# Kernel tuning notes

Hardware: AMD Instinct MI355X
Metric: run time of the kernel (lower is better)

Reference implementation:

```python
import jax, jax.numpy as jnp
import numpy as np

NEUMANN_TERMS = 6
EPS_PASSTHROUGH = 1e-6  # hn_config.GRADIENT_PASSTHROUGH_EPSILON (assumed)


def _cayley_neumann(W, terms=NEUMANN_TERMS):
    """Cayley transform U = (I - A)^{-1} (I + A) with A = skew(W),
    where (I - A)^{-1} is approximated by the truncated Neumann series
    sum_{k=0}^{terms-1} A^k."""
    A = 0.5 * (W - W.T)                       # skew-symmetric generator
    I = jnp.eye(W.shape[0], dtype=W.dtype)
    S = I
    P = I
    for _ in range(terms - 1):                # small fixed loop (neumann_terms)
        P = P @ A
        S = S + P
    return S @ (I + A)


def _quantum_rotation(h, theta):
    """Parametric quantum rotation activation: rotate adjacent feature pairs
    by angle theta (norm-preserving, replaces ReLU/GELU)."""
    N, d = h.shape
    hp = h.reshape(N, d // 2, 2)
    c, s = jnp.cos(theta), jnp.sin(theta)
    x0, x1 = hp[..., 0], hp[..., 1]
    r0 = c * x0 - s * x1
    r1 = s * x0 + c * x1
    return jnp.stack([r0, r1], axis=-1).reshape(N, d)


def setup_inputs() -> dict:
    key = jax.random.key(0)
    k1, k2, k3 = jax.random.split(key, 3)
    N, d_model, d_ff = 65536, 1024, 1024
    inputs = jax.random.normal(k1, (N, d_model), dtype=jnp.float32)
    # Orthogonal initializer with gain 0.1 (as in build())
    q1 = jnp.linalg.qr(jax.random.normal(k2, (d_ff, d_model), dtype=jnp.float32))[0]
    q2 = jnp.linalg.qr(jax.random.normal(k3, (d_model, d_ff), dtype=jnp.float32))[0]
    u1_weights = 0.1 * q1
    u2_weights = 0.1 * q2
    activation_angle = jnp.float32(0.7854)  # pi/4 initializer
    return {"inputs": inputs, "u1_weights": u1_weights,
            "u2_weights": u2_weights, "activation_angle": activation_angle}


def reference(inputs, u1_weights, u2_weights, activation_angle):
    U1 = _cayley_neumann(u1_weights)          # [d_ff, d_model]
    U2 = _cayley_neumann(u2_weights)          # [d_model, d_ff]
    h = inputs @ U1.T                         # [N, d_ff]
    h = _quantum_rotation(h, activation_angle)
    out = h @ U2.T                            # [N, d_model]
    # gradient passthrough term from call()
    passthrough = (jnp.mean(u1_weights) * EPS_PASSTHROUGH
                   + jnp.mean(u2_weights) * EPS_PASSTHROUGH
                   + activation_angle * EPS_PASSTHROUGH)
    return out + passthrough
```

## Files before the change

kernel.cpp:

```cpp
#include <hip/hip_runtime.h>
#include <hip/hip_bf16.h>
#include <stdint.h>


#define MM (1024 * 1024)

typedef __attribute__((ext_vector_type(4))) float f32x4;
typedef __attribute__((ext_vector_type(8))) short bf16x8;

__device__ __forceinline__ ushort f2bf(float f) {
  uint32_t u = __builtin_bit_cast(uint32_t, f);
  u += 0x7FFFu + ((u >> 16) & 1u);
  return (ushort)(u >> 16);
}

__device__ __forceinline__ void gld_lds16(const ushort* g, ushort* l) {
  __builtin_amdgcn_global_load_lds(
      (const __attribute__((address_space(1))) unsigned int*)g,
      (__attribute__((address_space(3))) unsigned int*)l, 16, 0, 0);
}

#define STAGE(GS, LB, BUF, H, KT)                                    \
  do {                                                               \
    const ushort* g_ = (GS) + (size_t)((H)*128) * K + (size_t)(KT)*64; \
    ushort* d_ = (LB) + (BUF)*32768 + (H)*128 * 64;                  \
    gld_lds16(g_, d_);                                               \
    gld_lds16(g_ + (size_t)64 * K, d_ + 64 * 64);                    \
  } while (0)

#define LDA(MH, BUF)                                                    \
  do {                                                                  \
    _Pragma("unroll") for (int ti = 0; ti < 4; ++ti) {                  \
      const ushort* p_ = rdA + (BUF)*32768 + ((MH)*64 + ti * 16 + lr) * 64; \
      af[ti][0] = *(const bf16x8*)(p_ + (pcol0 >> 1));                  \
      af[ti][1] = *(const bf16x8*)(p_ + (pcol1 >> 1));                  \
    }                                                                   \
  } while (0)

#define LDB(NH, BUF)                                                    \
  do {                                                                  \
    _Pragma("unroll") for (int tj = 0; tj < 2; ++tj) {                  \
      const ushort* p_ = rdB + (BUF)*32768 + ((NH)*32 + tj * 16 + lr) * 64; \
      bfr[tj][0] = *(const bf16x8*)(p_ + (pcol0 >> 1));                 \
      bfr[tj][1] = *(const bf16x8*)(p_ + (pcol1 >> 1));                 \
    }                                                                   \
  } while (0)

#define MFMA16(MH, NH)                                                  \
  do {                                                                  \
    __builtin_amdgcn_s_setprio(1);                                      \
    _Pragma("unroll") for (int m_ = 0; m_ < 4; ++m_)                    \
    _Pragma("unroll") for (int n_ = 0; n_ < 2; ++n_)                    \
    _Pragma("unroll") for (int ks_ = 0; ks_ < 2; ++ks_)                 \
      acc[(MH)*4 + m_][(NH)*2 + n_] =                                   \
          __builtin_amdgcn_mfma_f32_16x16x32_bf16(                      \
              af[m_][ks_], bfr[n_][ks_], acc[(MH)*4 + m_][(NH)*2 + n_], \
              0, 0, 0);                                                 \
    __builtin_amdgcn_s_setprio(0);                                      \
  } while (0)

#define CFENCE asm volatile("" ::: "memory")
#define SBAR                                  \
  do {                                        \
    CFENCE;                                   \
    __builtin_amdgcn_s_barrier();             \
    __builtin_amdgcn_sched_barrier(0);        \
  } while (0)

__global__ __launch_bounds__(512, 2) void gemm256(
    const ushort* __restrict__ X, const ushort* __restrict__ Y,
    float* __restrict__ o32, ushort* __restrict__ o16, int M, int N, int K,
    int mode, const float* __restrict__ theta_p,
    const float* __restrict__ sums) {
  extern __shared__ ushort lds[];

  const int tid = threadIdx.x;
  const int wave = tid >> 6, lane = tid & 63;

  const int nwg = gridDim.x * gridDim.y;
  const int lin = blockIdx.y * gridDim.x + blockIdx.x;
  const int wgid = (lin & 7) * (nwg >> 3) + (lin >> 3);
  const int bn = wgid & 3;
  const int bm = wgid >> 2;

  const int wrow = wave >> 2;
  const int wcol = wave & 3;

  const int srow = wave * 8 + (lane >> 3);
  const int scol = (((lane & 7) ^ ((lane >> 3) & 7)) << 3);
  const ushort* Xs = X + (size_t)(bm * 256 + srow) * K + scol;
  const ushort* Ys = Y + (size_t)(bn * 256 + srow) * K + scol;
  ushort* stA = lds + wave * 8 * 64;
  ushort* stB = lds + 16384 + wave * 8 * 64;

  const int lr = lane & 15;
  const int kqb = (lane >> 4) << 4;
  const int swz = (lr & 7) << 4;
  const int pcol0 = (0 + kqb) ^ swz;
  const int pcol1 = (64 + kqb) ^ swz;
  const ushort* rdA = lds + wrow * 128 * 64;
  const ushort* rdB = lds + 16384 + wcol * 64 * 64;

  f32x4 acc[8][4] = {};
  bf16x8 af[4][2], bfr[2][2];

  const int NT = K >> 6;

  STAGE(Xs, stA, 0, 0, 0);
  STAGE(Xs, stA, 0, 1, 0);
  STAGE(Ys, stB, 0, 0, 0);
  STAGE(Ys, stB, 0, 1, 0);

  for (int t = 0; t < NT; ++t) {
    const int cur = t & 1, nxt = cur ^ 1;
    const bool pf = (t + 1 < NT);
    if (pf) {
      STAGE(Xs, stA, nxt, 0, t + 1);
      asm volatile("s_waitcnt vmcnt(2)" ::: "memory");
    } else {
      asm volatile("s_waitcnt vmcnt(0)" ::: "memory");
    }
    SBAR;
    LDA(0, cur);
    LDB(0, cur);
    MFMA16(0, 0);
    SBAR;
    LDB(1, cur);
    if (pf) STAGE(Xs, stA, nxt, 1, t + 1);
    SBAR;
    MFMA16(0, 1);
    SBAR;
    LDA(1, cur);
    if (pf) STAGE(Ys, stB, nxt, 0, t + 1);
    SBAR;
    MFMA16(1, 1);
    SBAR;
    LDB(0, cur);
    if (pf) STAGE(Ys, stB, nxt, 1, t + 1);
    SBAR;
    MFMA16(1, 0);
    SBAR;
  }

  const int q4 = (lane >> 4) * 4;
  const int rbase = bm * 256 + wrow * 128;
  const int cbase = bn * 256 + wcol * 64;
  if (mode == 1) {
    float th = *theta_p, s, c;
    __sincosf(th, &s, &c);
    const float ssgn = (lane & 1) ? s : -s;
#pragma unroll
    for (int fi = 0; fi < 8; ++fi)
#pragma unroll
      for (int r = 0; r < 4; ++r) {
        const size_t row = (size_t)(rbase + fi * 16 + q4 + r);
        ushort* Orow = o16 + row * N;
#pragma unroll
        for (int fj = 0; fj < 4; ++fj) {
          float v = acc[fi][fj][r];
          float w = __shfl_xor(v, 1);
          Orow[cbase + fj * 16 + lr] = f2bf(c * v + ssgn * w);
        }
      }
  } else {
    const float pt = 1e-6f * (sums[0] * (1.0f / 1048576.0f) +
                              sums[1] * (1.0f / 1048576.0f) + *theta_p);
#pragma unroll
    for (int fi = 0; fi < 8; ++fi)
#pragma unroll
      for (int r = 0; r < 4; ++r) {
        const size_t row = (size_t)(rbase + fi * 16 + q4 + r);
        float* Orow = o32 + row * N;
#pragma unroll
        for (int fj = 0; fj < 4; ++fj)
          Orow[cbase + fj * 16 + lr] = acc[fi][fj][r] + pt;
      }
  }
}

__global__ __launch_bounds__(256, 2) void gemm_bt(
    const ushort* __restrict__ X0, const ushort* __restrict__ X1,
    const ushort* __restrict__ Y0, const ushort* __restrict__ Y1,
    float* __restrict__ o32, ushort* __restrict__ o16,
    ushort* __restrict__ o16b, const float* __restrict__ aux, int M, int N,
    int K, int mode, const float* __restrict__ theta_p,
    const float* __restrict__ sums) {
  __shared__ ushort lA[128 * 32];
  __shared__ ushort lB[128 * 32];

  const int tid = threadIdx.x;
  const int wave = tid >> 6, lane = tid & 63;
  const int bz = blockIdx.z;
  const int job = bz >> 1, mi = bz & 1;

  const int nwg = gridDim.x * gridDim.y;
  const int lin = blockIdx.y * gridDim.x + blockIdx.x;
  const int swzb = (lin & 7) * (nwg >> 3) + (lin >> 3);
  const int bn = swzb & 7;
  const int bm = swzb >> 3;

  const ushort* X = (job ? X1 : X0) + (size_t)mi * MM;
  const ushort* Y = (job ? Y1 : Y0) + (size_t)mi * MM;

  const ushort* Xg = X + (size_t)(bm * 128 + (tid >> 2)) * K + (tid & 3) * 8;
  const ushort* Yg = Y + (size_t)(bn * 128 + (tid >> 2)) * K + (tid & 3) * 8;
  ushort* lAw = lA + wave * 512;
  ushort* lBw = lB + wave * 512;

  const int wm = (wave & 1) * 64;
  const int wn = (wave >> 1) * 64;
  const int lr = lane & 15;
  const int kq = (lane >> 4) * 8;

  f32x4 acc[4][4] = {};

  for (int k0 = 0; k0 < K; k0 += 32) {
    __syncthreads();
    gld_lds16(Xg + k0, lAw);
    gld_lds16(Xg + k0 + (size_t)64 * K, lAw + 64 * 32);
    gld_lds16(Yg + k0, lBw);
    gld_lds16(Yg + k0 + (size_t)64 * K, lBw + 64 * 32);
    __syncthreads();

    bf16x8 afv[4], bfg[4];
#pragma unroll
    for (int t = 0; t < 4; ++t) {
      afv[t] = *(const bf16x8*)(lA + (wm + t * 16 + lr) * 32 + kq);
      bfg[t] = *(const bf16x8*)(lB + (wn + t * 16 + lr) * 32 + kq);
    }
#pragma unroll
    for (int ti = 0; ti < 4; ++ti)
#pragma unroll
      for (int tj = 0; tj < 4; ++tj)
        acc[ti][tj] = __builtin_amdgcn_mfma_f32_16x16x32_bf16(
            afv[ti], bfg[tj], acc[ti][tj], 0, 0, 0);
  }

  const int q4 = (lane >> 4) * 4;
  float* O = o32 + (size_t)bz * MM;
  ushort* P0 = (mode >= 3) ? o16 + (size_t)bz * MM : nullptr;
  ushort* P1 = (mode == 4) ? o16b + (size_t)bz * MM : nullptr;
  const float* Ax = (mode == 4) ? aux + (size_t)bz * MM : nullptr;
#pragma unroll
  for (int ti = 0; ti < 4; ++ti)
#pragma unroll
    for (int r = 0; r < 4; ++r) {
      const int row = bm * 128 + wm + ti * 16 + q4 + r;
      const size_t base = (size_t)row * N;
#pragma unroll
      for (int tj = 0; tj < 4; ++tj) {
        const int col = bn * 128 + wn + tj * 16 + lr;
        const float v = acc[ti][tj][r];
        O[base + col] = v;
        if (mode == 3) {
          P0[base + col] = f2bf(-v);
        } else if (mode == 4) {
          P0[base + col] = f2bf(v);
          const float diag = (row == col) ? 1.f : 0.f;
          P1[base + col] = f2bf(diag - Ax[base + col] + v);
        }
      }
    }
}

__global__ __launch_bounds__(256) void prep_a(const float* __restrict__ W1,
                                              const float* __restrict__ W2,
                                              ushort* __restrict__ Abf,
                                              float* __restrict__ sums) {
  __shared__ float sT[32][33];
  const int z = blockIdx.z;
  const float* W = z ? W2 : W1;
  ushort* A = Abf + (size_t)z * MM;
  const int r0 = blockIdx.y * 32, c0 = blockIdx.x * 32;
  const int x = threadIdx.x, y = threadIdx.y;

#pragma unroll
  for (int k = 0; k < 4; ++k)
    sT[y + 8 * k][x] = W[(size_t)(c0 + y + 8 * k) * 1024 + r0 + x];
  __syncthreads();

  float lsum = 0.f;
#pragma unroll
  for (int k = 0; k < 4; ++k) {
    int i = y + 8 * k;
    float w = W[(size_t)(r0 + i) * 1024 + c0 + x];
    lsum += w;
    A[(size_t)(r0 + i) * 1024 + c0 + x] = f2bf(0.5f * (w - sT[x][i]));
  }
#pragma unroll
  for (int off = 32; off > 0; off >>= 1) lsum += __shfl_down(lsum, off);
  if (((y * 32 + x) & 63) == 0) atomicAdd(&sums[z], lsum);
}

__global__ __launch_bounds__(256) void cvt_x(const float* __restrict__ x,
                                             ushort* __restrict__ xb) {
  const size_t i = (size_t)blockIdx.x * 256 + threadIdx.x;
  float4 v = ((const float4*)x)[i];
  ushort4 o;
  o.x = f2bf(v.x);
  o.y = f2bf(v.y);
  o.z = f2bf(v.z);
  o.w = f2bf(v.w);
  ((ushort4*)xb)[i] = o;
}

__global__ __launch_bounds__(256) void ew(const float* __restrict__ S1,
                                          const float* __restrict__ S2,
                                          const float* __restrict__ S3,
                                          const float* __restrict__ S4,
                                          ushort* __restrict__ O0) {
  const int idx = blockIdx.x * 256 + threadIdx.x;
  const int local = idx & (MM - 1);
  const float diag = ((local >> 10) == (local & 1023)) ? 1.f : 0.f;
  O0[idx] =
      f2bf(diag - 2.f * S1[idx] + 2.f * S2[idx] + 2.f * S3[idx] + S4[idx]);
}

extern "C" void kernel_launch(void* const* d_in, const int* in_sizes, int n_in,
                              void* d_out, int out_size, void* d_ws,
                              size_t ws_size, hipStream_t stream) {
  const float* xin = (const float*)d_in[0];
  const float* w1 = (const float*)d_in[1];
  const float* w2 = (const float*)d_in[2];
  const float* th = (const float*)d_in[3];
  float* out = (float*)d_out;

  char* w = (char*)d_ws;
  float* sums = (float*)w;
  ushort* Abf = (ushort*)(w + 256);
  ushort* Bbf = Abf + 2 * MM;
  ushort* B2bf = Bbf + 2 * MM;
  ushort* Fbf = B2bf + 2 * MM;
  ushort* Ubf = Fbf + 2 * MM;
  float* S1 = (float*)(Ubf + 2 * MM);
  float* S2 = S1 + 2 * MM;
  float* S34 = S2 + 2 * MM;
  ushort* xbf = (ushort*)(S34 + 4 * MM);
  ushort* hbf = xbf + (size_t)65536 * 1024;

  static bool inited = false;
  if (!inited) {
    (void)hipFuncSetAttribute((const void*)gemm256,
                              hipFuncAttributeMaxDynamicSharedMemorySize,
                              131072);
    inited = true;
  }

  hipMemsetAsync(sums, 0, 2 * sizeof(float), stream);

  prep_a<<<dim3(32, 32, 2), dim3(32, 8), 0, stream>>>(w1, w2, Abf, sums);
  cvt_x<<<65536, 256, 0, stream>>>(xin, xbf);

  gemm_bt<<<dim3(8, 8, 2), 256, 0, stream>>>(Abf, Abf, Abf, Abf, S1, Bbf,
                                             nullptr, nullptr, 1024, 1024,
                                             1024, 3, th, sums);
  gemm_bt<<<dim3(8, 8, 2), 256, 0, stream>>>(Bbf, Bbf, Bbf, Bbf, S2, B2bf, Fbf,
                                             S1, 1024, 1024, 1024, 4, th,
                                             sums);
  gemm_bt<<<dim3(8, 8, 4), 256, 0, stream>>>(Abf, B2bf, Fbf, Bbf, S34, nullptr,
                                             nullptr, nullptr, 1024, 1024,
                                             1024, 0, th, sums);
  ew<<<8192, 256, 0, stream>>>(S1, S2, S34, S34 + 2 * MM, Ubf);

  gemm256<<<dim3(4, 256, 1), 512, 131072, stream>>>(
      xbf, Ubf, nullptr, hbf, 65536, 1024, 1024, 1, th, sums);
  gemm256<<<dim3(4, 256, 1), 512, 131072, stream>>>(
      hbf, Ubf + MM, out, nullptr, 65536, 1024, 1024, 2, th, sums);
}
```

Measured before the change: 913.6 us.

## Refactor Neumann weight GEMM chain to one product and batch gemm256 prefetch

The Cayley/Neumann weight construction is re-expressed algebraically so the final U comes from a single product G·F, with the identity and scale terms folded into the GEMM epilogues. This drops one 4-batch GEMM, the elementwise combine kernel and several fp32 intermediates. Separately, the main 256-tile GEMM now issues all next-tile global-to-LDS loads at the top of each iteration instead of interleaving them between MFMA phases. That gives the loads more lead time but bunches memory traffic into one burst per iteration.

```diff
diff --git a/kernel.cpp b/kernel.cpp
--- a/kernel.cpp
+++ b/kernel.cpp
@@ -13,6 +13,10 @@
   u += 0x7FFFu + ((u >> 16) & 1u);
   return (ushort)(u >> 16);
 }
+__device__ __forceinline__ float bf2f(ushort h) {
+  uint32_t u = ((uint32_t)h) << 16;
+  return __builtin_bit_cast(float, u);
+}
 
 __device__ __forceinline__ void gld_lds16(const ushort* g, ushort* l) {
   __builtin_amdgcn_global_load_lds(
@@ -20,30 +24,30 @@
       (__attribute__((address_space(3))) unsigned int*)l, 16, 0, 0);
 }
 
-#define STAGE(GS, LB, BUF, H, KT)                                    \
-  do {                                                               \
+#define STAGE(GS, LB, BUF, H, KT)                                      \
+  do {                                                                 \
     const ushort* g_ = (GS) + (size_t)((H)*128) * K + (size_t)(KT)*64; \
-    ushort* d_ = (LB) + (BUF)*32768 + (H)*128 * 64;                  \
-    gld_lds16(g_, d_);                                               \
-    gld_lds16(g_ + (size_t)64 * K, d_ + 64 * 64);                    \
-  } while (0)
-
-#define LDA(MH, BUF)                                                    \
-  do {                                                                  \
-    _Pragma("unroll") for (int ti = 0; ti < 4; ++ti) {                  \
+    ushort* d_ = (LB) + (BUF)*32768 + (H)*128 * 64;                    \
+    gld_lds16(g_, d_);                                                 \
+    gld_lds16(g_ + (size_t)64 * K, d_ + 64 * 64);                      \
+  } while (0)
+
+#define LDA(MH, BUF)                                                        \
+  do {                                                                      \
+    _Pragma("unroll") for (int ti = 0; ti < 4; ++ti) {                      \
       const ushort* p_ = rdA + (BUF)*32768 + ((MH)*64 + ti * 16 + lr) * 64; \
-      af[ti][0] = *(const bf16x8*)(p_ + (pcol0 >> 1));                  \
-      af[ti][1] = *(const bf16x8*)(p_ + (pcol1 >> 1));                  \
-    }                                                                   \
-  } while (0)
-
-#define LDB(NH, BUF)                                                    \
-  do {                                                                  \
-    _Pragma("unroll") for (int tj = 0; tj < 2; ++tj) {                  \
+      af[ti][0] = *(const bf16x8*)(p_ + (pcol0 >> 1));                      \
+      af[ti][1] = *(const bf16x8*)(p_ + (pcol1 >> 1));                      \
+    }                                                                       \
+  } while (0)
+
+#define LDB(NH, BUF)                                                        \
+  do {                                                                      \
+    _Pragma("unroll") for (int tj = 0; tj < 2; ++tj) {                      \
       const ushort* p_ = rdB + (BUF)*32768 + ((NH)*32 + tj * 16 + lr) * 64; \
-      bfr[tj][0] = *(const bf16x8*)(p_ + (pcol0 >> 1));                 \
-      bfr[tj][1] = *(const bf16x8*)(p_ + (pcol1 >> 1));                 \
-    }                                                                   \
+      bfr[tj][0] = *(const bf16x8*)(p_ + (pcol0 >> 1));                     \
+      bfr[tj][1] = *(const bf16x8*)(p_ + (pcol1 >> 1));                     \
+    }                                                                       \
   } while (0)
 
 #define MFMA16(MH, NH)                                                  \
@@ -60,11 +64,11 @@
   } while (0)
 
 #define CFENCE asm volatile("" ::: "memory")
-#define SBAR                                  \
-  do {                                        \
-    CFENCE;                                   \
-    __builtin_amdgcn_s_barrier();             \
-    __builtin_amdgcn_sched_barrier(0);        \
+#define SBAR                           \
+  do {                                 \
+    CFENCE;                            \
+    __builtin_amdgcn_s_barrier();      \
+    __builtin_amdgcn_sched_barrier(0); \
   } while (0)
 
 __global__ __launch_bounds__(512, 2) void gemm256(
@@ -113,10 +117,12 @@
 
   for (int t = 0; t < NT; ++t) {
     const int cur = t & 1, nxt = cur ^ 1;
-    const bool pf = (t + 1 < NT);
-    if (pf) {
+    if (t + 1 < NT) {
       STAGE(Xs, stA, nxt, 0, t + 1);
-      asm volatile("s_waitcnt vmcnt(2)" ::: "memory");
+      STAGE(Xs, stA, nxt, 1, t + 1);
+      STAGE(Ys, stB, nxt, 0, t + 1);
+      STAGE(Ys, stB, nxt, 1, t + 1);
+      asm volatile("s_waitcnt vmcnt(8)" ::: "memory");
     } else {
       asm volatile("s_waitcnt vmcnt(0)" ::: "memory");
     }
@@ -126,17 +132,14 @@
     MFMA16(0, 0);
     SBAR;
     LDB(1, cur);
-    if (pf) STAGE(Xs, stA, nxt, 1, t + 1);
     SBAR;
     MFMA16(0, 1);
     SBAR;
     LDA(1, cur);
-    if (pf) STAGE(Ys, stB, nxt, 0, t + 1);
     SBAR;
     MFMA16(1, 1);
     SBAR;
     LDB(0, cur);
-    if (pf) STAGE(Ys, stB, nxt, 1, t + 1);
     SBAR;
     MFMA16(1, 0);
     SBAR;
@@ -179,19 +182,17 @@
 }
 
 __global__ __launch_bounds__(256, 2) void gemm_bt(
-    const ushort* __restrict__ X0, const ushort* __restrict__ X1,
-    const ushort* __restrict__ Y0, const ushort* __restrict__ Y1,
+    const ushort* __restrict__ X0, const ushort* __restrict__ Y0,
     float* __restrict__ o32, ushort* __restrict__ o16,
-    ushort* __restrict__ o16b, const float* __restrict__ aux, int M, int N,
-    int K, int mode, const float* __restrict__ theta_p,
-    const float* __restrict__ sums) {
+    ushort* __restrict__ o16b, const float* __restrict__ auxf,
+    const ushort* __restrict__ auxb, int M, int N, int K, int mode,
+    const float* __restrict__ theta_p, const float* __restrict__ sums) {
   __shared__ ushort lA[128 * 32];
   __shared__ ushort lB[128 * 32];
 
   const int tid = threadIdx.x;
   const int wave = tid >> 6, lane = tid & 63;
-  const int bz = blockIdx.z;
-  const int job = bz >> 1, mi = bz & 1;
+  const int mi = blockIdx.z & 1;
 
   const int nwg = gridDim.x * gridDim.y;
   const int lin = blockIdx.y * gridDim.x + blockIdx.x;
@@ -199,8 +200,8 @@
   const int bn = swzb & 7;
   const int bm = swzb >> 3;
 
-  const ushort* X = (job ? X1 : X0) + (size_t)mi * MM;
-  const ushort* Y = (job ? Y1 : Y0) + (size_t)mi * MM;
+  const ushort* X = X0 + (size_t)mi * MM;
+  const ushort* Y = Y0 + (size_t)mi * MM;
 
   const ushort* Xg = X + (size_t)(bm * 128 + (tid >> 2)) * K + (tid & 3) * 8;
   const ushort* Yg = Y + (size_t)(bn * 128 + (tid >> 2)) * K + (tid & 3) * 8;
@@ -237,10 +238,12 @@
   }
 
   const int q4 = (lane >> 4) * 4;
-  float* O = o32 + (size_t)bz * MM;
-  ushort* P0 = (mode >= 3) ? o16 + (size_t)bz * MM : nullptr;
-  ushort* P1 = (mode == 4) ? o16b + (size_t)bz * MM : nullptr;
-  const float* Ax = (mode == 4) ? aux + (size_t)bz * MM : nullptr;
+  const size_t zoff = (size_t)mi * MM;
+  float* O = (mode == 3) ? o32 + zoff : nullptr;
+  ushort* P0 = o16 + zoff;
+  ushort* P1 = (mode == 3) ? o16b + zoff : nullptr;
+  const float* Ax = (mode == 4) ? auxf + zoff : nullptr;
+  const ushort* Ab = (mode == 3) ? auxb + zoff : nullptr;
 #pragma unroll
   for (int ti = 0; ti < 4; ++ti)
 #pragma unroll
@@ -251,13 +254,15 @@
       for (int tj = 0; tj < 4; ++tj) {
         const int col = bn * 128 + wn + tj * 16 + lr;
         const float v = acc[ti][tj][r];
-        O[base + col] = v;
+        const float diag = (row == col) ? 1.f : 0.f;
         if (mode == 3) {
+          O[base + col] = v;
           P0[base + col] = f2bf(-v);
+          P1[base + col] = f2bf(diag + 2.f * bf2f(Ab[base + col]) - v);
         } else if (mode == 4) {
+          P0[base + col] = f2bf(diag - Ax[base + col] + v);
+        } else {
           P0[base + col] = f2bf(v);
-          const float diag = (row == col) ? 1.f : 0.f;
-          P1[base + col] = f2bf(diag - Ax[base + col] + v);
         }
       }
     }
@@ -304,18 +309,6 @@
   ((ushort4*)xb)[i] = o;
 }
 
-__global__ __launch_bounds__(256) void ew(const float* __restrict__ S1,
-                                          const float* __restrict__ S2,
-                                          const float* __restrict__ S3,
-                                          const float* __restrict__ S4,
-                                          ushort* __restrict__ O0) {
-  const int idx = blockIdx.x * 256 + threadIdx.x;
-  const int local = idx & (MM - 1);
-  const float diag = ((local >> 10) == (local & 1023)) ? 1.f : 0.f;
-  O0[idx] =
-      f2bf(diag - 2.f * S1[idx] + 2.f * S2[idx] + 2.f * S3[idx] + S4[idx]);
-}
-
 extern "C" void kernel_launch(void* const* d_in, const int* in_sizes, int n_in,
                               void* d_out, int out_size, void* d_ws,
                               size_t ws_size, hipStream_t stream) {
@@ -329,13 +322,11 @@
   float* sums = (float*)w;
   ushort* Abf = (ushort*)(w + 256);
   ushort* Bbf = Abf + 2 * MM;
-  ushort* B2bf = Bbf + 2 * MM;
-  ushort* Fbf = B2bf + 2 * MM;
+  ushort* Gbf = Bbf + 2 * MM;
+  ushort* Fbf = Gbf + 2 * MM;
   ushort* Ubf = Fbf + 2 * MM;
   float* S1 = (float*)(Ubf + 2 * MM);
-  float* S2 = S1 + 2 * MM;
-  float* S34 = S2 + 2 * MM;
-  ushort* xbf = (ushort*)(S34 + 4 * MM);
+  ushort* xbf = (ushort*)(S1 + 2 * MM);
   ushort* hbf = xbf + (size_t)65536 * 1024;
 
   static bool inited = false;
@@ -351,16 +342,15 @@
   prep_a<<<dim3(32, 32, 2), dim3(32, 8), 0, stream>>>(w1, w2, Abf, sums);
   cvt_x<<<65536, 256, 0, stream>>>(xin, xbf);
 
-  gemm_bt<<<dim3(8, 8, 2), 256, 0, stream>>>(Abf, Abf, Abf, Abf, S1, Bbf,
+  gemm_bt<<<dim3(8, 8, 2), 256, 0, stream>>>(Abf, Abf, S1, Bbf, Gbf, nullptr,
+                                             Abf, 1024, 1024, 1024, 3, th,
+                                             sums);
+  gemm_bt<<<dim3(8, 8, 2), 256, 0, stream>>>(Bbf, Bbf, nullptr, Fbf, nullptr,
+                                             S1, nullptr, 1024, 1024, 1024, 4,
+                                             th, sums);
+  gemm_bt<<<dim3(8, 8, 2), 256, 0, stream>>>(Gbf, Fbf, nullptr, Ubf, nullptr,
                                              nullptr, nullptr, 1024, 1024,
-                                             1024, 3, th, sums);
-  gemm_bt<<<dim3(8, 8, 2), 256, 0, stream>>>(Bbf, Bbf, Bbf, Bbf, S2, B2bf, Fbf,
-                                             S1, 1024, 1024, 1024, 4, th,
-                                             sums);
-  gemm_bt<<<dim3(8, 8, 4), 256, 0, stream>>>(Abf, B2bf, Fbf, Bbf, S34, nullptr,
-                                             nullptr, nullptr, 1024, 1024,
-                                             1024, 0, th, sums);
-  ew<<<8192, 256, 0, stream>>>(S1, S2, S34, S34 + 2 * MM, Ubf);
+                                             1024, 5, th, sums);
 
   gemm256<<<dim3(4, 256, 1), 512, 131072, stream>>>(
       xbf, Ubf, nullptr, hbf, 65536, 1024, 1024, 1, th, sums);
```

After: 959.4 us. 1.05x slower.
